# Kernel optimization log

Hardware: AMD Instinct MI355X
Metric: run time of the kernel (lower is better)

The kernel has to match this reference:

```python
import jax, jax.numpy as jnp
import numpy as np

H = 384
W = 384
C_X = 64       # channels of x (== out_channels)
C_PTX = 64     # channels of ptx
C_IN = C_X + C_PTX  # Linear in_channels = 128
C_OUT = 64
N_TGT = 120000  # number of target pixels (CSR segments)
DEG = 8         # points per target pixel
N_PTS = N_TGT * DEG


def setup_inputs() -> dict:
    key = jax.random.key(0)
    k1, k2, k3, k4 = jax.random.split(key, 4)
    x = jax.random.normal(k1, (1, C_X, H, W), jnp.float32)
    ptx = jax.random.normal(k2, (N_PTS, C_PTX), jnp.float32)
    # CSR row pointer over points per target pixel (monotone, ends at N_PTS)
    point_key = jnp.arange(N_TGT + 1, dtype=jnp.int32) * DEG
    # unique target-pixel indices into H*W
    pixel_tgt_idx = jnp.arange(N_TGT, dtype=jnp.int32)
    sm_w = jax.random.normal(k3, (C_IN, 1), jnp.float32) * 0.05
    sm_b = jnp.zeros((1,), jnp.float32)
    fo_w = jax.random.normal(k4, (C_IN, C_OUT), jnp.float32) * 0.05
    fo_b = jnp.zeros((C_OUT,), jnp.float32)
    return {"x": x, "ptx": ptx, "sm_w": sm_w, "sm_b": sm_b,
            "fo_w": fo_w, "fo_b": fo_b, "point_key": point_key,
            "pixel_tgt_idx": pixel_tgt_idx, "bs": 1, "height": H, "width": W}


def reference(x, ptx, sm_w, sm_b, fo_w, fo_b, point_key, pixel_tgt_idx, bs, height, width):
    # segment id per point from CSR rowptr (static total length for jit)
    seg = jnp.repeat(jnp.arange(N_TGT, dtype=jnp.int32), jnp.diff(point_key),
                     total_repeat_length=N_PTS)
    # pixel features gathered to target pixels, then CSR-gathered to points
    feat_px = x.transpose(0, 2, 3, 1).reshape(height * width, C_X)[pixel_tgt_idx]
    feat = jnp.concatenate([ptx, feat_px[seg]], axis=1)  # [N_PTS, C_IN]
    # _net_forward: identity (base class)
    # segment softmax over points within each pixel group
    logits = feat @ sm_w + sm_b  # [N_PTS, 1]
    m = jax.ops.segment_max(logits, seg, num_segments=N_TGT)
    e = jnp.exp(logits - m[seg])
    s = jax.ops.segment_sum(e, seg, num_segments=N_TGT)
    weight = e / (s[seg] + 1e-16)
    # feat_out projection replaces ptx
    ptx_out = feat @ fo_w + fo_b  # [N_PTS, C_OUT]
    agg = jax.ops.segment_sum(weight * ptx_out, seg, num_segments=N_TGT)  # [N_TGT, C_OUT]
    # list_to_map: scatter aggregated features back to image grid + mask
    flat = jnp.zeros((height * width, C_OUT), x.dtype).at[pixel_tgt_idx].set(agg)
    mask = jnp.zeros((height * width, 1), x.dtype).at[pixel_tgt_idx].set(1.0)
    fmap = flat.reshape(1, height, width, C_OUT).transpose(0, 3, 1, 2)
    mmap = mask.reshape(1, height, width, 1).transpose(0, 3, 1, 2)
    x_out = jnp.where(mmap > 0, fmap, x)
    return x_out, ptx_out
```

## Files before the change

kernel.cpp:

```cpp
#include <hip/hip_runtime.h>
#include <hip/hip_bf16.h>
#include <math.h>

typedef __attribute__((ext_vector_type(8))) short short8v;
typedef __attribute__((ext_vector_type(4))) short short4v;
typedef __attribute__((ext_vector_type(4))) float float4v;

#define TB 64

__device__ __forceinline__ short f2bf(float f) {
    __hip_bfloat16 h = __float2bfloat16(f);
    short s; __builtin_memcpy(&s, &h, sizeof(short));
    return s;
}
__device__ __forceinline__ float bf2f(short u) {
    unsigned int x = ((unsigned int)(unsigned short)u) << 16;
    float f; __builtin_memcpy(&f, &x, sizeof(float));
    return f;
}
__device__ __forceinline__ float4v mfma_bf16(short8v a, short8v b, float4v c) {
    return __builtin_amdgcn_mfma_f32_16x16x32_bf16(a, b, c, 0, 0, 0);
}

__global__ __launch_bounds__(256)
void copy_x_kernel(const float4* __restrict__ x, float4* __restrict__ out, int n4) {
    int i = blockIdx.x * blockDim.x + threadIdx.x;
    if (i < n4) out[i] = x[i];
}

__global__ __launch_bounds__(256)
void prep_w_kernel(const float* __restrict__ fo_w, const float* __restrict__ sm_w,
                   unsigned short* __restrict__ ws) {
    int t = blockIdx.x * 256 + threadIdx.x;
    if (t >= 18 * 64) return;
    const int frag = t >> 6, lane = t & 63;
    const int lo16 = lane & 15, g = lane >> 4;
    short8v v;
    if (frag < 16) {
        const int isB2 = frag >> 3, f = frag & 7;
        const int ct = f >> 1, kh = f & 1;
        const int kbase = isB2 * 64 + kh * 32 + g * 8;
        const int col = ct * 16 + lo16;
        #pragma unroll
        for (int j = 0; j < 8; ++j)
            v[j] = f2bf(fo_w[(size_t)(kbase + j) * 64 + col]);
    } else {
        const int kh = frag & 1;
        #pragma unroll
        for (int j = 0; j < 8; ++j)
            v[j] = f2bf(sm_w[kh * 32 + g * 8 + j]);
    }
    *(short8v*)&ws[(size_t)t * 8] = v;
}

__global__ __launch_bounds__(256, 4)
void fused_kernel(const float* __restrict__ x,
                  const float* __restrict__ ptx,
                  const unsigned short* __restrict__ ws,
                  const float* __restrict__ fo_b,
                  const int* __restrict__ point_key,
                  const int* __restrict__ pixel_tgt_idx,
                  float* __restrict__ xout,
                  float* __restrict__ ptx_out,
                  int n_tgt, int n_pts, int hw)
{
    __shared__ __align__(16) unsigned short sraw[64 * 72];
    __shared__ __align__(16) unsigned short agg_b[64][72];
    __shared__ int pix_s[TB], r0_s[TB], deg_s[TB];
    unsigned short (*fpx)[72]   = (unsigned short (*)[72])sraw;
    unsigned short (*q_lds)[72] = (unsigned short (*)[72])sraw;

    const int tid  = threadIdx.x;
    const int lane = tid & 63;
    const int w    = tid >> 6;
    const int lo16 = lane & 15;
    const int g    = lane >> 4;
    const int t0   = blockIdx.x * TB;
    const int tw0  = w * 16;

    if (tid < TB) {
        int t = t0 + tid;
        bool v = t < n_tgt;
        int r0 = v ? point_key[t] : 0;
        int d  = v ? (point_key[t + 1] - r0) : 0;
        pix_s[tid] = v ? pixel_tgt_idx[t] : 0;
        r0_s[tid]  = r0;
        deg_s[tid] = d > 8 ? 8 : d;
    }
    __syncthreads();

    int pgm[8];
    #pragma unroll
    for (int mt = 0; mt < 8; ++mt) {
        int tlA = tw0 + mt * 2 + (lo16 >> 3);
        int pg  = r0_s[tlA] + (lo16 & 7);
        pgm[mt] = pg < n_pts ? pg : n_pts - 1;
    }

    {
        const int tgt = tid >> 2, q4 = tid & 3;
        const int pix = pix_s[tgt];
        const float* xp = x + (size_t)(q4 * 16) * hw + pix;
        #pragma unroll
        for (int hhalf = 0; hhalf < 2; ++hhalf) {
            short8v pk;
            #pragma unroll
            for (int j = 0; j < 8; ++j)
                pk[j] = f2bf(xp[(size_t)(hhalf * 8 + j) * hw]);
            *(short8v*)&fpx[tgt][q4 * 16 + hhalf * 8] = pk;
        }
    }

    short8v b1[5][2];
    #pragma unroll
    for (int ct = 0; ct < 4; ++ct)
        #pragma unroll
        for (int kh = 0; kh < 2; ++kh)
            b1[ct][kh] = *(const short8v*)&ws[(size_t)((ct * 2 + kh) * 64 + lane) * 8];
    #pragma unroll
    for (int kh = 0; kh < 2; ++kh)
        b1[4][kh] = *(const short8v*)&ws[(size_t)((16 + kh) * 64 + lane) * 8];

    float4 lb0, lb1, lb2, lb3;
    {
        const float* prow = ptx + (size_t)pgm[0] * 64 + g * 8;
        lb0 = *(const float4*)(prow);
        lb1 = *(const float4*)(prow + 4);
        lb2 = *(const float4*)(prow + 32);
        lb3 = *(const float4*)(prow + 36);
    }

    float4v qv4[4];
    {
        short8v a20 = *(const short8v*)&fpx[tw0 + lo16][g * 8];
        short8v a21 = *(const short8v*)&fpx[tw0 + lo16][32 + g * 8];
        #pragma unroll
        for (int ct = 0; ct < 4; ++ct) {
            short8v b20 = *(const short8v*)&ws[(size_t)((8 + ct * 2 + 0) * 64 + lane) * 8];
            short8v b21 = *(const short8v*)&ws[(size_t)((8 + ct * 2 + 1) * 64 + lane) * 8];
            float4v z = {0.f, 0.f, 0.f, 0.f};
            z = mfma_bf16(b20, a20, z);
            qv4[ct] = mfma_bf16(b21, a21, z);
        }
    }
    {
        float4 fb40 = *(const float4*)&fo_b[ 0 + g * 4];
        float4 fb41 = *(const float4*)&fo_b[16 + g * 4];
        float4 fb42 = *(const float4*)&fo_b[32 + g * 4];
        float4 fb43 = *(const float4*)&fo_b[48 + g * 4];
        short4v q0, q1, q2, q3;
        q0[0] = f2bf(qv4[0][0] + fb40.x); q0[1] = f2bf(qv4[0][1] + fb40.y);
        q0[2] = f2bf(qv4[0][2] + fb40.z); q0[3] = f2bf(qv4[0][3] + fb40.w);
        q1[0] = f2bf(qv4[1][0] + fb41.x); q1[1] = f2bf(qv4[1][1] + fb41.y);
        q1[2] = f2bf(qv4[1][2] + fb41.z); q1[3] = f2bf(qv4[1][3] + fb41.w);
        q2[0] = f2bf(qv4[2][0] + fb42.x); q2[1] = f2bf(qv4[2][1] + fb42.y);
        q2[2] = f2bf(qv4[2][2] + fb42.z); q2[3] = f2bf(qv4[2][3] + fb42.w);
        q3[0] = f2bf(qv4[3][0] + fb43.x); q3[1] = f2bf(qv4[3][1] + fb43.y);
        q3[2] = f2bf(qv4[3][2] + fb43.z); q3[3] = f2bf(qv4[3][3] + fb43.w);
        *(short4v*)&q_lds[tw0 + lo16][ 0 + g * 4] = q0;
        *(short4v*)&q_lds[tw0 + lo16][16 + g * 4] = q1;
        *(short4v*)&q_lds[tw0 + lo16][32 + g * 4] = q2;
        *(short4v*)&q_lds[tw0 + lo16][48 + g * 4] = q3;
    }

#define EPIL_CT(CT, CREG)                                                      \
    {                                                                          \
        const int colb = (CT) * 16 + g * 4;                                    \
        const short4v qb = *(const short4v*)&q_lds[tE][colb];                  \
        float4v po;                                                            \
        po[0] = CREG[0] + bf2f(qb[0]); po[1] = CREG[1] + bf2f(qb[1]);          \
        po[2] = CREG[2] + bf2f(qb[2]); po[3] = CREG[3] + bf2f(qb[3]);          \
        if (val)                                                               \
            *(float4v*)&ptx_out[(size_t)(r0E + pE) * 64 + colb] = po;          \
        float s0 = po[0] * wn, s1 = po[1] * wn, s2 = po[2] * wn, s3 = po[3] * wn; \
        s0 += __shfl_xor(s0, 1); s1 += __shfl_xor(s1, 1);                      \
        s2 += __shfl_xor(s2, 1); s3 += __shfl_xor(s3, 1);                      \
        s0 += __shfl_xor(s0, 2); s1 += __shfl_xor(s1, 2);                      \
        s2 += __shfl_xor(s2, 2); s3 += __shfl_xor(s3, 2);                      \
        s0 += __shfl_xor(s0, 4); s1 += __shfl_xor(s1, 4);                      \
        s2 += __shfl_xor(s2, 4); s3 += __shfl_xor(s3, 4);                      \
        if (pE == 0) {                                                         \
            short4v ag;                                                        \
            ag[0] = f2bf(s0); ag[1] = f2bf(s1);                                \
            ag[2] = f2bf(s2); ag[3] = f2bf(s3);                                \
            *(short4v*)&agg_b[tE][colb] = ag;                                  \
        }                                                                      \
    }

    #pragma unroll
    for (int mt = 0; mt < 8; ++mt) {
        short8v a0, a1;
        a0[0] = f2bf(lb0.x); a0[1] = f2bf(lb0.y); a0[2] = f2bf(lb0.z); a0[3] = f2bf(lb0.w);
        a0[4] = f2bf(lb1.x); a0[5] = f2bf(lb1.y); a0[6] = f2bf(lb1.z); a0[7] = f2bf(lb1.w);
        a1[0] = f2bf(lb2.x); a1[1] = f2bf(lb2.y); a1[2] = f2bf(lb2.z); a1[3] = f2bf(lb2.w);
        a1[4] = f2bf(lb3.x); a1[5] = f2bf(lb3.y); a1[6] = f2bf(lb3.z); a1[7] = f2bf(lb3.w);

        if (mt < 7) {
            const float* prow = ptx + (size_t)pgm[mt + 1] * 64 + g * 8;
            lb0 = *(const float4*)(prow);
            lb1 = *(const float4*)(prow + 4);
            lb2 = *(const float4*)(prow + 32);
            lb3 = *(const float4*)(prow + 36);
        }

        float4v z = {0.f, 0.f, 0.f, 0.f};
        float4v cc0 = mfma_bf16(b1[0][1], a1, mfma_bf16(b1[0][0], a0, z));
        float4v cc1 = mfma_bf16(b1[1][1], a1, mfma_bf16(b1[1][0], a0, z));
        float4v cc2 = mfma_bf16(b1[2][1], a1, mfma_bf16(b1[2][0], a0, z));
        float4v cc3 = mfma_bf16(b1[3][1], a1, mfma_bf16(b1[3][0], a0, z));
        float4v cc4 = mfma_bf16(b1[4][1], a1, mfma_bf16(b1[4][0], a0, z));

        const int tE   = tw0 + mt * 2 + (lo16 >> 3);
        const int degE = deg_s[tE];
        const int r0E  = r0_s[tE];
        const int pE   = lo16 & 7;
        const bool val = (pE < degE);

        float lg = val ? cc4[0] : -3.4e38f;
        float mx = lg;
        mx = fmaxf(mx, __shfl_xor(mx, 1));
        mx = fmaxf(mx, __shfl_xor(mx, 2));
        mx = fmaxf(mx, __shfl_xor(mx, 4));
        float e = val ? __expf(lg - mx) : 0.0f;
        float sm = e;
        sm += __shfl_xor(sm, 1);
        sm += __shfl_xor(sm, 2);
        sm += __shfl_xor(sm, 4);
        const float wn = e / (sm + 1e-16f);

        EPIL_CT(0, cc0)
        EPIL_CT(1, cc1)
        EPIL_CT(2, cc2)
        EPIL_CT(3, cc3)
    }
#undef EPIL_CT

    {
        const int tgt = tid >> 2, q4 = tid & 3;
        if (t0 + tgt < n_tgt) {
            const int pix = pix_s[tgt];
            float* xp = xout + (size_t)(q4 * 16) * hw + pix;
            #pragma unroll
            for (int u = 0; u < 4; ++u) {
                short4v v = *(const short4v*)&agg_b[tgt][q4 * 16 + u * 4];
                xp[(size_t)(u * 4 + 0) * hw] = bf2f(v[0]);
                xp[(size_t)(u * 4 + 1) * hw] = bf2f(v[1]);
                xp[(size_t)(u * 4 + 2) * hw] = bf2f(v[2]);
                xp[(size_t)(u * 4 + 3) * hw] = bf2f(v[3]);
            }
        }
    }
}

extern "C" void kernel_launch(void* const* d_in, const int* in_sizes, int n_in,
                              void* d_out, int out_size, void* d_ws, size_t ws_size,
                              hipStream_t stream) {
    const float* x             = (const float*)d_in[0];
    const float* ptx           = (const float*)d_in[1];
    const float* sm_w          = (const float*)d_in[2];
    const float* fo_w          = (const float*)d_in[4];
    const float* fo_b          = (const float*)d_in[5];
    const int*   point_key     = (const int*)d_in[6];
    const int*   pixel_tgt_idx = (const int*)d_in[7];

    const int x_elems = in_sizes[0];
    const int hw      = x_elems / 64;
    const int n_tgt   = in_sizes[7];
    const int n_pts   = in_sizes[1] / 64;

    float* xout    = (float*)d_out;
    float* ptx_out = xout + (size_t)x_elems;

    const int n4 = x_elems / 4;
    copy_x_kernel<<<(n4 + 255) / 256, 256, 0, stream>>>(
        (const float4*)x, (float4*)xout, n4);

    prep_w_kernel<<<5, 256, 0, stream>>>(fo_w, sm_w, (unsigned short*)d_ws);

    const int blocks = (n_tgt + TB - 1) / TB;
    fused_kernel<<<blocks, 256, 0, stream>>>(
        x, ptx, (const unsigned short*)d_ws, fo_b, point_key, pixel_tgt_idx,
        xout, ptx_out, n_tgt, n_pts, hw);
}
```

Baseline: 140.0 us.

## Copy only non-target pixels of x inside the fused kernel via a mask

Result: no change. 140.9 us (+0.7%).

```diff
diff --git a/kernel.cpp b/kernel.cpp
--- a/kernel.cpp
+++ b/kernel.cpp
@@ -7,6 +7,7 @@
 typedef __attribute__((ext_vector_type(4))) float float4v;
 
 #define TB 64
+#define WS_MASK_OFF 32768
 
 __device__ __forceinline__ short f2bf(float f) {
     __hip_bfloat16 h = __float2bfloat16(f);
@@ -23,7 +24,13 @@
 }
 
 __global__ __launch_bounds__(256)
-void copy_x_kernel(const float4* __restrict__ x, float4* __restrict__ out, int n4) {
+void mask_set_kernel(const int* __restrict__ idx, unsigned char* __restrict__ mask, int n) {
+    int i = blockIdx.x * blockDim.x + threadIdx.x;
+    if (i < n) mask[idx[i]] = 1;
+}
+
+__global__ __launch_bounds__(256)
+void copy_x_kernel(const float4v* __restrict__ x, float4v* __restrict__ out, int n4) {
     int i = blockIdx.x * blockDim.x + threadIdx.x;
     if (i < n4) out[i] = x[i];
 }
@@ -62,7 +69,8 @@
                   const int* __restrict__ pixel_tgt_idx,
                   float* __restrict__ xout,
                   float* __restrict__ ptx_out,
-                  int n_tgt, int n_pts, int hw)
+                  const unsigned int* __restrict__ mask4,
+                  int n_tgt, int n_pts, int hw, int q4n, int fusedBlocks)
 {
     __shared__ __align__(16) unsigned short sraw[64 * 72];
     __shared__ __align__(16) unsigned short agg_b[64][72];
@@ -70,7 +78,20 @@
     unsigned short (*fpx)[72]   = (unsigned short (*)[72])sraw;
     unsigned short (*q_lds)[72] = (unsigned short (*)[72])sraw;
 
-    const int tid  = threadIdx.x;
+    const int tid = threadIdx.x;
+
+    if ((int)blockIdx.x >= fusedBlocks) {
+        const int i = (blockIdx.x - fusedBlocks) * 256 + tid;
+        if (i < q4n && mask4[i] != 0x01010101u) {
+            const float4v* x4 = (const float4v*)x;
+            float4v* o4 = (float4v*)xout;
+            #pragma unroll 4
+            for (int c = 0; c < 64; ++c)
+                o4[(size_t)c * q4n + i] = x4[(size_t)c * q4n + i];
+        }
+        return;
+    }
+
     const int lane = tid & 63;
     const int w    = tid >> 6;
     const int lo16 = lane & 15;
@@ -271,14 +292,29 @@
     float* xout    = (float*)d_out;
     float* ptx_out = xout + (size_t)x_elems;
 
-    const int n4 = x_elems / 4;
-    copy_x_kernel<<<(n4 + 255) / 256, 256, 0, stream>>>(
-        (const float4*)x, (float4*)xout, n4);
-
     prep_w_kernel<<<5, 256, 0, stream>>>(fo_w, sm_w, (unsigned short*)d_ws);
 
-    const int blocks = (n_tgt + TB - 1) / TB;
-    fused_kernel<<<blocks, 256, 0, stream>>>(
-        x, ptx, (const unsigned short*)d_ws, fo_b, point_key, pixel_tgt_idx,
-        xout, ptx_out, n_tgt, n_pts, hw);
-}
+    const int fusedBlocks = (n_tgt + TB - 1) / TB;
+    const int q4n = hw / 4;
+    const bool maskOK = (ws_size >= (size_t)WS_MASK_OFF + (size_t)hw) && ((hw & 3) == 0);
+
+    if (maskOK) {
+        unsigned char* mask = (unsigned char*)d_ws + WS_MASK_OFF;
+        hipMemsetAsync(mask, 0, (size_t)hw, stream);
+        mask_set_kernel<<<(n_tgt + 255) / 256, 256, 0, stream>>>(
+            pixel_tgt_idx, mask, n_tgt);
+        const int copyBlocks = (q4n + 255) / 256;
+        fused_kernel<<<fusedBlocks + copyBlocks, 256, 0, stream>>>(
+            x, ptx, (const unsigned short*)d_ws, fo_b, point_key, pixel_tgt_idx,
+            xout, ptx_out, (const unsigned int*)mask,
+            n_tgt, n_pts, hw, q4n, fusedBlocks);
+    } else {
+        const int n4 = x_elems / 4;
+        copy_x_kernel<<<(n4 + 255) / 256, 256, 0, stream>>>(
+            (const float4v*)x, (float4v*)xout, n4);
+        fused_kernel<<<fusedBlocks, 256, 0, stream>>>(
+            x, ptx, (const unsigned short*)d_ws, fo_b, point_key, pixel_tgt_idx,
+            xout, ptx_out, (const unsigned int*)d_ws,
+            n_tgt, n_pts, hw, q4n, fusedBlocks);
+    }
+}
```
